# Optimization experiments

Measured on AMD Instinct MI355X. Metric: run time of the kernel, lower is better.

## Reference

```python
import jax, jax.numpy as jnp
import numpy as np

N_ENT = 200000
N_REL = 500
D_MODEL = 512
BS = 256


def setup_inputs() -> dict:
    key = jax.random.key(0)
    k1, k2, k3, k4, k5, k6 = jax.random.split(key, 6)
    return {
        "s_ent": jax.random.randint(k1, (BS,), 0, N_ENT, dtype=jnp.int32),
        "relation": jax.random.randint(k2, (BS,), 0, N_REL, dtype=jnp.int32),
        "o_ent": jax.random.randint(k3, (BS,), 0, N_ENT, dtype=jnp.int32),
        "time": jax.random.randint(k4, (BS,), 0, 365, dtype=jnp.int32),
        "ent_emb": jax.random.normal(k5, (N_ENT, D_MODEL), dtype=jnp.float32),
        "rel_emb": jax.random.normal(k6, (N_REL, D_MODEL), dtype=jnp.float32),
    }


def reference(s_ent, relation, o_ent, time, ent_emb, rel_emb):
    # test_forward: scores = -||(e_s + r) - E_all||_2 for every entity.
    # Faithful math via the ||a-b||^2 = ||a||^2 - 2 a.b + ||b||^2 GEMM
    # decomposition, avoiding the [bs, n_ent, d] difference tensor.
    cond = ent_emb[s_ent] + rel_emb[relation]          # [bs, d]
    a2 = jnp.sum(cond * cond, axis=-1, keepdims=True)  # [bs, 1]
    b2 = jnp.sum(ent_emb * ent_emb, axis=-1)           # [n_ent]
    ab = jnp.einsum('bd,nd->bn', cond, ent_emb)        # [bs, n_ent]
    d2 = a2 - 2.0 * ab + b2[None, :]
    scores = -jnp.sqrt(jnp.maximum(d2, 1e-12))
    return scores
```

## Files before the change

kernel.cpp:

```cpp
#include <hip/hip_runtime.h>
#include <hip/hip_bf16.h>

typedef __attribute__((ext_vector_type(8))) short short8;
typedef __attribute__((ext_vector_type(4))) float f32x4;

#define D_MODEL 512
#define BN 128
#define BK 32
#define NSTEPS (D_MODEL / BK)

__device__ inline short f2bf(float f) {
    unsigned u = __builtin_bit_cast(unsigned, f);
    unsigned r = (u + 0x7fffu + ((u >> 16) & 1u)) >> 16;
    return (short)r;
}

__global__ void prep_kernel(const int* __restrict__ s_ent, const int* __restrict__ rel,
                            const float* __restrict__ ent, const float* __restrict__ relemb,
                            short* __restrict__ condb, float* __restrict__ a2) {
    const int b = blockIdx.x;
    const int t = threadIdx.x;
    const float4 v = *(const float4*)(ent + (size_t)s_ent[b] * D_MODEL + t * 4);
    const float4 w = *(const float4*)(relemb + (size_t)rel[b] * D_MODEL + t * 4);
    float c0 = v.x + w.x, c1 = v.y + w.y, c2 = v.z + w.z, c3 = v.w + w.w;
    float sq = c0 * c0 + c1 * c1 + c2 * c2 + c3 * c3;

    short4 s;
    s.x = f2bf(c0); s.y = f2bf(c1); s.z = f2bf(c2); s.w = f2bf(c3);
    *(short4*)(condb + (size_t)b * D_MODEL + t * 4) = s;

    #pragma unroll
    for (int off = 1; off < 64; off <<= 1) sq += __shfl_xor(sq, off);
    __shared__ float red[2];
    if ((t & 63) == 0) red[t >> 6] = sq;
    __syncthreads();
    if (t == 0) a2[b] = red[0] + red[1];
}

__global__ __launch_bounds__(512, 4)
void score_kernel(const float* __restrict__ ent, const short* __restrict__ condb,
                  const float* __restrict__ a2, float* __restrict__ out, const int n_ent) {
    __shared__ __align__(16) short Bl[2][BN * 40];
    __shared__ float b2s[BN];

    const int tid  = threadIdx.x;
    const int lane = tid & 63;
    const int w    = tid >> 6;
    const int wm   = w >> 1;
    const int wn   = w & 1;
    const int lrow = lane & 15;
    const int lk   = (lane >> 4) * 8;
    const int nbase = blockIdx.x * BN;

    const int sr = tid >> 2;
    const int sk = (tid & 3) * 8;
    const bool rvalid = (nbase + sr) < n_ent;
    const float* gsrc = ent + (size_t)(nbase + sr) * D_MODEL + sk;

    f32x4 acc[4][4] = {};
    float sq = 0.f;

    float4 p0 = {0.f, 0.f, 0.f, 0.f}, p1 = {0.f, 0.f, 0.f, 0.f};
    if (rvalid) { p0 = *(const float4*)(gsrc); p1 = *(const float4*)(gsrc + 4); }

    #pragma unroll 2
    for (int t = 0; t < NSTEPS; ++t) {
        sq += p0.x * p0.x + p0.y * p0.y + p0.z * p0.z + p0.w * p0.w
            + p1.x * p1.x + p1.y * p1.y + p1.z * p1.z + p1.w * p1.w;
        short8 bs;
        bs[0] = f2bf(p0.x); bs[1] = f2bf(p0.y); bs[2] = f2bf(p0.z); bs[3] = f2bf(p0.w);
        bs[4] = f2bf(p1.x); bs[5] = f2bf(p1.y); bs[6] = f2bf(p1.z); bs[7] = f2bf(p1.w);
        *(short8*)(&Bl[t & 1][sr * 40 + sk]) = bs;

        if (t < NSTEPS - 1 && rvalid) {
            p0 = *(const float4*)(gsrc + (t + 1) * BK);
            p1 = *(const float4*)(gsrc + (t + 1) * BK + 4);
        }

        __syncthreads();

        const short* abase = condb + (size_t)(wm * 64 + lrow) * D_MODEL + t * BK + lk;
        short8 af[4];
        #pragma unroll
        for (int fm = 0; fm < 4; ++fm) af[fm] = *(const short8*)(abase + fm * 16 * D_MODEL);

        #pragma unroll
        for (int fn = 0; fn < 4; ++fn) {
            short8 bfv = *(const short8*)(&Bl[t & 1][(wn * 64 + fn * 16 + lrow) * 40 + lk]);
            #pragma unroll
            for (int fm = 0; fm < 4; ++fm)
                acc[fm][fn] = __builtin_amdgcn_mfma_f32_16x16x32_bf16(af[fm], bfv, acc[fm][fn], 0, 0, 0);
        }
    }

    sq += __shfl_xor(sq, 1);
    sq += __shfl_xor(sq, 2);
    if ((tid & 3) == 0) b2s[sr] = sq;
    __syncthreads();

    #pragma unroll
    for (int fm = 0; fm < 4; ++fm) {
        const int m = wm * 64 + fm * 16 + (lane >> 4) * 4;
        const f32x4 a2v = *(const f32x4*)(a2 + m);
        #pragma unroll
        for (int fn = 0; fn < 4; ++fn) {
            const int nl = wn * 64 + fn * 16 + lrow;
            const int ng = nbase + nl;
            if (ng < n_ent) {
                const float b2v = b2s[nl];
                #pragma unroll
                for (int r = 0; r < 4; ++r) {
                    float d2 = a2v[r] - 2.f * acc[fm][fn][r] + b2v;
                    out[(size_t)(m + r) * n_ent + ng] = -sqrtf(fmaxf(d2, 1e-12f));
                }
            }
        }
    }
}

extern "C" void kernel_launch(void* const* d_in, const int* in_sizes, int n_in,
                              void* d_out, int out_size, void* d_ws, size_t ws_size,
                              hipStream_t stream) {
    const int*   s_ent  = (const int*)d_in[0];
    const int*   rel    = (const int*)d_in[1];
    const float* ent    = (const float*)d_in[4];
    const float* relemb = (const float*)d_in[5];
    float* out = (float*)d_out;

    const int bs    = in_sizes[0];
    const int n_ent = in_sizes[4] / D_MODEL;

    short* condb = (short*)d_ws;
    float* a2    = (float*)((char*)d_ws + (size_t)bs * D_MODEL * 2);

    prep_kernel<<<bs, 128, 0, stream>>>(s_ent, rel, ent, relemb, condb, a2);

    const int ntiles = (n_ent + BN - 1) / BN;
    score_kernel<<<ntiles, 512, 0, stream>>>(ent, condb, a2, out, n_ent);
}
```

Baseline: 202.1 us.

## Stream A and fp32 B tiles to LDS via async global_load_lds with multi-buffering

The score kernel now copies both the bf16 query tile and the raw fp32 entity tile straight from global memory into swizzled LDS with async global_load_lds. A is double-buffered and B is triple-buffered, and waits use explicit vmcnt counters so loads for later k-steps overlap the MFMA work. The bf16 conversion and the squared-norm accumulation move to after the LDS read, so each wave converts its own B fragments. This duplicates conversion work across the wm waves and raises LDS use to about 80KB per block, which likely lowers the number of resident blocks per CU.

```diff
diff --git a/kernel.cpp b/kernel.cpp
--- a/kernel.cpp
+++ b/kernel.cpp
@@ -6,10 +6,17 @@
 
 #define D_MODEL 512
 #define BN 128
-#define BK 32
-#define NSTEPS (D_MODEL / BK)
+#define NT 16
+#define A_TILE 16384
+#define B_TILE 16384
 
-__device__ inline short f2bf(float f) {
+__device__ __forceinline__ void gload16(const void* gptr, void* lptr) {
+    typedef const __attribute__((address_space(1))) unsigned GT;
+    typedef __attribute__((address_space(3))) unsigned LT;
+    __builtin_amdgcn_global_load_lds((GT*)gptr, (LT*)lptr, 16, 0, 0);
+}
+
+__device__ __forceinline__ short f2bf(float f) {
     unsigned u = __builtin_bit_cast(unsigned, f);
     unsigned r = (u + 0x7fffu + ((u >> 16) & 1u)) >> 16;
     return (short)r;
@@ -40,68 +47,106 @@
 __global__ __launch_bounds__(512, 4)
 void score_kernel(const float* __restrict__ ent, const short* __restrict__ condb,
                   const float* __restrict__ a2, float* __restrict__ out, const int n_ent) {
-    __shared__ __align__(16) short Bl[2][BN * 40];
-    __shared__ float b2s[BN];
+    __shared__ __align__(16) unsigned char lds[2 * A_TILE + 3 * B_TILE];
+    unsigned char* Al = lds;
+    unsigned char* Bl = lds + 2 * A_TILE;
 
     const int tid  = threadIdx.x;
     const int lane = tid & 63;
-    const int w    = tid >> 6;
-    const int wm   = w >> 1;
-    const int wn   = w & 1;
-    const int lrow = lane & 15;
-    const int lk   = (lane >> 4) * 8;
+    const int w    = tid >> 6, wm = w >> 1, wn = w & 1;
+    const int lrow = lane & 15, g4 = lane >> 4;
     const int nbase = blockIdx.x * BN;
 
-    const int sr = tid >> 2;
-    const int sk = (tid & 3) * 8;
-    const bool rvalid = (nbase + sr) < n_ent;
-    const float* gsrc = ent + (size_t)(nbase + sr) * D_MODEL + sk;
+    const int p0 = tid * 16, p1 = p0 + 8192;
+    const int ar0 = p0 >> 6, ar1 = p1 >> 6;
+    const char* gA0 = (const char*)condb + ar0 * 1024 + ((p0 & 63) ^ ((ar0 & 3) << 4));
+    const char* gA1 = (const char*)condb + ar1 * 1024 + ((p1 & 63) ^ ((ar1 & 3) << 4));
+    const int br0 = p0 >> 7, br1 = p1 >> 7;
+    const long long gr0 = min(nbase + br0, n_ent - 1);
+    const long long gr1 = min(nbase + br1, n_ent - 1);
+    const char* gB0 = (const char*)ent + gr0 * 2048 + ((p0 & 127) ^ ((br0 & 7) << 4));
+    const char* gB1 = (const char*)ent + gr1 * 2048 + ((p1 & 127) ^ ((br1 & 7) << 4));
+
+    int aoff[4], boff0[4], boff1[4];
+    #pragma unroll
+    for (int f = 0; f < 4; ++f) {
+        const int ra = wm * 64 + f * 16 + lrow;
+        aoff[f] = ra * 64 + ((g4 * 16) ^ ((ra & 3) << 4));
+        const int rb = wn * 64 + f * 16 + lrow;
+        const int sw = (rb & 7) << 4;
+        boff0[f] = rb * 128 + ((g4 * 32) ^ sw);
+        boff1[f] = rb * 128 + ((g4 * 32 + 16) ^ sw);
+    }
 
     f32x4 acc[4][4] = {};
-    float sq = 0.f;
+    float sq[4] = {0.f, 0.f, 0.f, 0.f};
 
-    float4 p0 = {0.f, 0.f, 0.f, 0.f}, p1 = {0.f, 0.f, 0.f, 0.f};
-    if (rvalid) { p0 = *(const float4*)(gsrc); p1 = *(const float4*)(gsrc + 4); }
+    gload16(gA0, Al + p0);
+    gload16(gA1, Al + p1);
+    gload16(gB0, Bl + p0);
+    gload16(gB1, Bl + p1);
+    gload16(gB0 + 128, Bl + B_TILE + p0);
+    gload16(gB1 + 128, Bl + B_TILE + p1);
 
-    #pragma unroll 2
-    for (int t = 0; t < NSTEPS; ++t) {
-        sq += p0.x * p0.x + p0.y * p0.y + p0.z * p0.z + p0.w * p0.w
-            + p1.x * p1.x + p1.y * p1.y + p1.z * p1.z + p1.w * p1.w;
-        short8 bs;
-        bs[0] = f2bf(p0.x); bs[1] = f2bf(p0.y); bs[2] = f2bf(p0.z); bs[3] = f2bf(p0.w);
-        bs[4] = f2bf(p1.x); bs[5] = f2bf(p1.y); bs[6] = f2bf(p1.z); bs[7] = f2bf(p1.w);
-        *(short8*)(&Bl[t & 1][sr * 40 + sk]) = bs;
+    for (int t = 0; t < NT; ++t) {
+        if (t == NT - 1) { asm volatile("s_waitcnt vmcnt(0)" ::: "memory"); }
+        else             { asm volatile("s_waitcnt vmcnt(2)" ::: "memory"); }
+        __builtin_amdgcn_s_barrier();
 
-        if (t < NSTEPS - 1 && rvalid) {
-            p0 = *(const float4*)(gsrc + (t + 1) * BK);
-            p1 = *(const float4*)(gsrc + (t + 1) * BK + 4);
+        if (t + 1 < NT) {
+            unsigned char* ad = Al + ((t + 1) & 1) * A_TILE;
+            gload16(gA0 + (t + 1) * 64, ad + p0);
+            gload16(gA1 + (t + 1) * 64, ad + p1);
+        }
+        if (t + 2 < NT) {
+            unsigned char* bd = Bl + ((t + 2) % 3) * B_TILE;
+            gload16(gB0 + (t + 2) * 128, bd + p0);
+            gload16(gB1 + (t + 2) * 128, bd + p1);
         }
 
-        __syncthreads();
+        const unsigned char* ab = Al + (t & 1) * A_TILE;
+        const unsigned char* bb = Bl + (t % 3) * B_TILE;
 
-        const short* abase = condb + (size_t)(wm * 64 + lrow) * D_MODEL + t * BK + lk;
         short8 af[4];
         #pragma unroll
-        for (int fm = 0; fm < 4; ++fm) af[fm] = *(const short8*)(abase + fm * 16 * D_MODEL);
+        for (int fm = 0; fm < 4; ++fm) af[fm] = *(const short8*)(ab + aoff[fm]);
 
         #pragma unroll
         for (int fn = 0; fn < 4; ++fn) {
-            short8 bfv = *(const short8*)(&Bl[t & 1][(wn * 64 + fn * 16 + lrow) * 40 + lk]);
+            const f32x4 v0 = *(const f32x4*)(bb + boff0[fn]);
+            const f32x4 v1 = *(const f32x4*)(bb + boff1[fn]);
+            if (wm == 0)
+                sq[fn] += v0[0]*v0[0] + v0[1]*v0[1] + v0[2]*v0[2] + v0[3]*v0[3]
+                        + v1[0]*v1[0] + v1[1]*v1[1] + v1[2]*v1[2] + v1[3]*v1[3];
+            union { __hip_bfloat162 h[4]; short8 s; } cv;
+            cv.h[0] = __float22bfloat162_rn(make_float2(v0[0], v0[1]));
+            cv.h[1] = __float22bfloat162_rn(make_float2(v0[2], v0[3]));
+            cv.h[2] = __float22bfloat162_rn(make_float2(v1[0], v1[1]));
+            cv.h[3] = __float22bfloat162_rn(make_float2(v1[2], v1[3]));
             #pragma unroll
             for (int fm = 0; fm < 4; ++fm)
-                acc[fm][fn] = __builtin_amdgcn_mfma_f32_16x16x32_bf16(af[fm], bfv, acc[fm][fn], 0, 0, 0);
+                acc[fm][fn] = __builtin_amdgcn_mfma_f32_16x16x32_bf16(af[fm], cv.s, acc[fm][fn], 0, 0, 0);
         }
     }
 
-    sq += __shfl_xor(sq, 1);
-    sq += __shfl_xor(sq, 2);
-    if ((tid & 3) == 0) b2s[sr] = sq;
+    float* b2s = (float*)lds;
+    if (wm == 0) {
+        #pragma unroll
+        for (int fn = 0; fn < 4; ++fn) {
+            sq[fn] += __shfl_xor(sq[fn], 16);
+            sq[fn] += __shfl_xor(sq[fn], 32);
+        }
+        if (lane < 16) {
+            #pragma unroll
+            for (int fn = 0; fn < 4; ++fn) b2s[wn * 64 + fn * 16 + lane] = sq[fn];
+        }
+    }
     __syncthreads();
 
     #pragma unroll
     for (int fm = 0; fm < 4; ++fm) {
-        const int m = wm * 64 + fm * 16 + (lane >> 4) * 4;
-        const f32x4 a2v = *(const f32x4*)(a2 + m);
+        const int m0 = wm * 64 + fm * 16 + g4 * 4;
+        const f32x4 a2v = *(const f32x4*)(a2 + m0);
         #pragma unroll
         for (int fn = 0; fn < 4; ++fn) {
             const int nl = wn * 64 + fn * 16 + lrow;
@@ -111,7 +156,7 @@
                 #pragma unroll
                 for (int r = 0; r < 4; ++r) {
                     float d2 = a2v[r] - 2.f * acc[fm][fn][r] + b2v;
-                    out[(size_t)(m + r) * n_ent + ng] = -sqrtf(fmaxf(d2, 1e-12f));
+                    out[(size_t)(m0 + r) * n_ent + ng] = -sqrtf(fmaxf(d2, 1e-12f));
                 }
             }
         }
```

After: 164.6 us. -18.6%, faster.

## Stage A tile via global_load_lds with swizzled LDS and deeper B prefetch

Applied to the files above, without the earlier changes.

Stages the bf16 condition matrix into LDS using direct global-to-LDS loads instead of having each wave fetch it from global memory every k-step. The entity rows are prefetched two k-steps ahead in registers, and B is stored in an XOR-swizzled LDS layout instead of the padded one. The k-loop is hand-unrolled with explicit waitcnt and barrier placement to overlap loads, conversion and MFMA work. The larger LDS footprint (48 KB per block) may reduce how many blocks fit on each CU. The b2 reduction buffer now reuses the tile LDS space.

```diff
diff --git a/kernel.cpp b/kernel.cpp
--- a/kernel.cpp
+++ b/kernel.cpp
@@ -6,13 +6,33 @@
 
 #define D_MODEL 512
 #define BN 128
-#define BK 32
-#define NSTEPS (D_MODEL / BK)
+#define NT 16
+#define A_TILE 16384
+#define B_TILE 8192
 
-__device__ inline short f2bf(float f) {
+__device__ __forceinline__ void gload16(const void* g, void* l) {
+    typedef const __attribute__((address_space(1))) unsigned GT;
+    typedef __attribute__((address_space(3))) unsigned LT;
+    __builtin_amdgcn_global_load_lds((GT*)g, (LT*)l, 16, 0, 0);
+}
+
+__device__ __forceinline__ short f2bf(float f) {
     unsigned u = __builtin_bit_cast(unsigned, f);
     unsigned r = (u + 0x7fffu + ((u >> 16) & 1u)) >> 16;
     return (short)r;
+}
+
+__device__ __forceinline__ short8 cvt8(const float4& a, const float4& b) {
+    union { __hip_bfloat162 h[4]; short8 s; } u;
+    u.h[0] = __float22bfloat162_rn(make_float2(a.x, a.y));
+    u.h[1] = __float22bfloat162_rn(make_float2(a.z, a.w));
+    u.h[2] = __float22bfloat162_rn(make_float2(b.x, b.y));
+    u.h[3] = __float22bfloat162_rn(make_float2(b.z, b.w));
+    return u.s;
+}
+__device__ __forceinline__ float ssq(const float4& a, const float4& b) {
+    return a.x*a.x + a.y*a.y + a.z*a.z + a.w*a.w
+         + b.x*b.x + b.y*b.y + b.z*b.z + b.w*b.w;
 }
 
 __global__ void prep_kernel(const int* __restrict__ s_ent, const int* __restrict__ rel,
@@ -40,68 +60,88 @@
 __global__ __launch_bounds__(512, 4)
 void score_kernel(const float* __restrict__ ent, const short* __restrict__ condb,
                   const float* __restrict__ a2, float* __restrict__ out, const int n_ent) {
-    __shared__ __align__(16) short Bl[2][BN * 40];
-    __shared__ float b2s[BN];
+    __shared__ __align__(16) unsigned char lds[2 * A_TILE + 2 * B_TILE];
+    unsigned char* Al = lds;
+    unsigned char* Bl = lds + 2 * A_TILE;
 
     const int tid  = threadIdx.x;
     const int lane = tid & 63;
-    const int w    = tid >> 6;
-    const int wm   = w >> 1;
-    const int wn   = w & 1;
-    const int lrow = lane & 15;
-    const int lk   = (lane >> 4) * 8;
+    const int w    = tid >> 6, wm = w >> 1, wn = w & 1;
+    const int lrow = lane & 15, g4 = lane >> 4;
     const int nbase = blockIdx.x * BN;
 
-    const int sr = tid >> 2;
-    const int sk = (tid & 3) * 8;
-    const bool rvalid = (nbase + sr) < n_ent;
-    const float* gsrc = ent + (size_t)(nbase + sr) * D_MODEL + sk;
+    const int p0 = tid * 16, p1 = p0 + 8192;
+    const int ar0 = p0 >> 6, ar1 = p1 >> 6;
+    const char* gA0 = (const char*)condb + ar0 * 1024 + ((p0 & 63) ^ ((ar0 & 3) << 4));
+    const char* gA1 = (const char*)condb + ar1 * 1024 + ((p1 & 63) ^ ((ar1 & 3) << 4));
+
+    const int sr = tid >> 2, sk = (tid & 3) * 8;
+    const long long gr = min((long long)(nbase + sr), (long long)(n_ent - 1));
+    const float* gB = ent + gr * D_MODEL + sk;
+    const int bwoff = sr * 64 + ((sk * 2) ^ ((sr & 3) << 4));
+
+    const int base_a = (wm * 64 + lrow) * 64 + ((g4 * 16) ^ ((lrow & 3) << 4));
+    const int base_b = (wn * 64 + lrow) * 64 + ((g4 * 16) ^ ((lrow & 3) << 4));
 
     f32x4 acc[4][4] = {};
     float sq = 0.f;
 
-    float4 p0 = {0.f, 0.f, 0.f, 0.f}, p1 = {0.f, 0.f, 0.f, 0.f};
-    if (rvalid) { p0 = *(const float4*)(gsrc); p1 = *(const float4*)(gsrc + 4); }
+    float4 rbA0 = *(const float4*)(gB);
+    float4 rbA1 = *(const float4*)(gB + 4);
+    float4 rbB0 = *(const float4*)(gB + 32);
+    float4 rbB1 = *(const float4*)(gB + 36);
+    gload16(gA0, Al + p0);
+    gload16(gA1, Al + p1);
+    sq += ssq(rbA0, rbA1);
+    *(short8*)(Bl + bwoff) = cvt8(rbA0, rbA1);
 
-    #pragma unroll 2
-    for (int t = 0; t < NSTEPS; ++t) {
-        sq += p0.x * p0.x + p0.y * p0.y + p0.z * p0.z + p0.w * p0.w
-            + p1.x * p1.x + p1.y * p1.y + p1.z * p1.z + p1.w * p1.w;
-        short8 bs;
-        bs[0] = f2bf(p0.x); bs[1] = f2bf(p0.y); bs[2] = f2bf(p0.z); bs[3] = f2bf(p0.w);
-        bs[4] = f2bf(p1.x); bs[5] = f2bf(p1.y); bs[6] = f2bf(p1.z); bs[7] = f2bf(p1.w);
-        *(short8*)(&Bl[t & 1][sr * 40 + sk]) = bs;
+#define KSTEP(T, CV0, CV1, LD0, LD1, DO_CVT, DO_LDB, DO_LDA)                              \
+  {                                                                                        \
+    asm volatile("s_waitcnt vmcnt(0)" ::: "memory");                                       \
+    short8 cb;                                                                             \
+    if (DO_CVT) { sq += ssq(CV0, CV1); cb = cvt8(CV0, CV1); }                              \
+    asm volatile("s_waitcnt lgkmcnt(0)" ::: "memory");                                     \
+    __builtin_amdgcn_s_barrier();                                                          \
+    if (DO_LDB) { LD0 = *(const float4*)(gB + ((T) + 2) * 32);                             \
+                  LD1 = *(const float4*)(gB + ((T) + 2) * 32 + 4); }                       \
+    if (DO_LDA) { unsigned char* ad = Al + (((T) + 1) & 1) * A_TILE;                       \
+                  gload16(gA0 + ((T) + 1) * 64, ad + p0);                                  \
+                  gload16(gA1 + ((T) + 1) * 64, ad + p1); }                                \
+    if (DO_CVT) *(short8*)(Bl + (((T) + 1) & 1) * B_TILE + bwoff) = cb;                    \
+    const unsigned char* ab = Al + ((T) & 1) * A_TILE;                                     \
+    const unsigned char* bb = Bl + ((T) & 1) * B_TILE;                                     \
+    short8 af0 = *(const short8*)(ab + base_a);                                            \
+    short8 af1 = *(const short8*)(ab + base_a + 1024);                                     \
+    short8 af2 = *(const short8*)(ab + base_a + 2048);                                     \
+    short8 af3 = *(const short8*)(ab + base_a + 3072);                                     \
+    _Pragma("unroll")                                                                      \
+    for (int fn = 0; fn < 4; ++fn) {                                                       \
+      short8 bf = *(const short8*)(bb + base_b + fn * 1024);                               \
+      acc[0][fn] = __builtin_amdgcn_mfma_f32_16x16x32_bf16(af0, bf, acc[0][fn], 0, 0, 0);  \
+      acc[1][fn] = __builtin_amdgcn_mfma_f32_16x16x32_bf16(af1, bf, acc[1][fn], 0, 0, 0);  \
+      acc[2][fn] = __builtin_amdgcn_mfma_f32_16x16x32_bf16(af2, bf, acc[2][fn], 0, 0, 0);  \
+      acc[3][fn] = __builtin_amdgcn_mfma_f32_16x16x32_bf16(af3, bf, acc[3][fn], 0, 0, 0);  \
+    }                                                                                      \
+  }
 
-        if (t < NSTEPS - 1 && rvalid) {
-            p0 = *(const float4*)(gsrc + (t + 1) * BK);
-            p1 = *(const float4*)(gsrc + (t + 1) * BK + 4);
-        }
-
-        __syncthreads();
-
-        const short* abase = condb + (size_t)(wm * 64 + lrow) * D_MODEL + t * BK + lk;
-        short8 af[4];
-        #pragma unroll
-        for (int fm = 0; fm < 4; ++fm) af[fm] = *(const short8*)(abase + fm * 16 * D_MODEL);
-
-        #pragma unroll
-        for (int fn = 0; fn < 4; ++fn) {
-            short8 bfv = *(const short8*)(&Bl[t & 1][(wn * 64 + fn * 16 + lrow) * 40 + lk]);
-            #pragma unroll
-            for (int fm = 0; fm < 4; ++fm)
-                acc[fm][fn] = __builtin_amdgcn_mfma_f32_16x16x32_bf16(af[fm], bfv, acc[fm][fn], 0, 0, 0);
-        }
+    for (int tt = 0; tt < 14; tt += 2) {
+        KSTEP(tt,     rbB0, rbB1, rbA0, rbA1, true,  true,  true)
+        KSTEP(tt + 1, rbA0, rbA1, rbB0, rbB1, true,  true,  true)
     }
+    KSTEP(14, rbB0, rbB1, rbA0, rbA1, true,  false, true)
+    KSTEP(15, rbA0, rbA1, rbB0, rbB1, false, false, false)
+#undef KSTEP
 
     sq += __shfl_xor(sq, 1);
     sq += __shfl_xor(sq, 2);
+    float* b2s = (float*)lds;
     if ((tid & 3) == 0) b2s[sr] = sq;
     __syncthreads();
 
     #pragma unroll
     for (int fm = 0; fm < 4; ++fm) {
-        const int m = wm * 64 + fm * 16 + (lane >> 4) * 4;
-        const f32x4 a2v = *(const f32x4*)(a2 + m);
+        const int m0 = wm * 64 + fm * 16 + g4 * 4;
+        const f32x4 a2v = *(const f32x4*)(a2 + m0);
         #pragma unroll
         for (int fn = 0; fn < 4; ++fn) {
             const int nl = wn * 64 + fn * 16 + lrow;
@@ -111,7 +151,7 @@
                 #pragma unroll
                 for (int r = 0; r < 4; ++r) {
                     float d2 = a2v[r] - 2.f * acc[fm][fn][r] + b2v;
-                    out[(size_t)(m + r) * n_ent + ng] = -sqrtf(fmaxf(d2, 1e-12f));
+                    out[(size_t)(m0 + r) * n_ent + ng] = -sqrtf(fmaxf(d2, 1e-12f));
                 }
             }
         }
```

New measurement: 173.7 us. 14.1% less time.

## Stage whole entity tile in swizzled LDS once, drop K-loop barriers

Applied to the files above, without the earlier changes.

The score kernel now uses 64-entity tiles. Each block issues all sixteen global loads per thread up front, converts the full 512-wide rows to bf16 with a packed conversion intrinsic, and writes them into an XOR-swizzled LDS buffer behind a single barrier. The MFMA loop then runs over K with no per-step synchronisation, and each wave covers 32 query rows across all 64 entities. This removes sixteen barriers and the serialized load/convert/compute pipeline, at the cost of 64KB of LDS per block, which can limit occupancy, and about twice as many A-fragment reloads from global memory per output.

```diff
diff --git a/kernel.cpp b/kernel.cpp
--- a/kernel.cpp
+++ b/kernel.cpp
@@ -5,14 +5,20 @@
 typedef __attribute__((ext_vector_type(4))) float f32x4;
 
 #define D_MODEL 512
-#define BN 128
-#define BK 32
-#define NSTEPS (D_MODEL / BK)
+#define BN 64
+#define NPASS 16
 
-__device__ inline short f2bf(float f) {
+__device__ __forceinline__ short f2bf(float f) {
     unsigned u = __builtin_bit_cast(unsigned, f);
     unsigned r = (u + 0x7fffu + ((u >> 16) & 1u)) >> 16;
     return (short)r;
+}
+
+__device__ __forceinline__ short4 cvt4(const float4& v) {
+    union { __hip_bfloat162 h[2]; short4 s; } u;
+    u.h[0] = __float22bfloat162_rn(make_float2(v.x, v.y));
+    u.h[1] = __float22bfloat162_rn(make_float2(v.z, v.w));
+    return u.s;
 }
 
 __global__ void prep_kernel(const int* __restrict__ s_ent, const int* __restrict__ rel,
@@ -40,78 +46,72 @@
 __global__ __launch_bounds__(512, 4)
 void score_kernel(const float* __restrict__ ent, const short* __restrict__ condb,
                   const float* __restrict__ a2, float* __restrict__ out, const int n_ent) {
-    __shared__ __align__(16) short Bl[2][BN * 40];
+    __shared__ __align__(16) short Bp[BN * D_MODEL];
     __shared__ float b2s[BN];
 
     const int tid  = threadIdx.x;
     const int lane = tid & 63;
     const int w    = tid >> 6;
-    const int wm   = w >> 1;
-    const int wn   = w & 1;
-    const int lrow = lane & 15;
-    const int lk   = (lane >> 4) * 8;
-    const int nbase = blockIdx.x * BN;
+    const int lrow = lane & 15, g4 = lane >> 4;
+    const long long nbase = (long long)blockIdx.x * BN;
 
-    const int sr = tid >> 2;
-    const int sk = (tid & 3) * 8;
-    const bool rvalid = (nbase + sr) < n_ent;
-    const float* gsrc = ent + (size_t)(nbase + sr) * D_MODEL + sk;
+    const char* gent = (const char*)ent;
+    float4 stg[NPASS];
+    #pragma unroll
+    for (int p = 0; p < NPASS; ++p) {
+        const long long grow = min(nbase + w * 8 + (p >> 1), (long long)(n_ent - 1));
+        stg[p] = *(const float4*)(gent + grow * 2048 + (p & 1) * 1024 + lane * 16);
+    }
+    float sqp[8];
+    #pragma unroll
+    for (int r = 0; r < 8; ++r) sqp[r] = 0.f;
+    #pragma unroll
+    for (int p = 0; p < NPASS; ++p) {
+        const int row = w * 8 + (p >> 1);
+        const int cb  = (p & 1) * 512 + lane * 8;
+        const float4 v = stg[p];
+        sqp[p >> 1] += v.x * v.x + v.y * v.y + v.z * v.z + v.w * v.w;
+        *(short4*)((char*)Bp + row * 1024 + (cb ^ ((row & 7) << 4))) = cvt4(v);
+    }
+    #pragma unroll
+    for (int r = 0; r < 8; ++r) {
+        float s = sqp[r];
+        #pragma unroll
+        for (int off = 1; off < 64; off <<= 1) s += __shfl_xor(s, off);
+        if (lane == 0) b2s[w * 8 + r] = s;
+    }
+    __syncthreads();
 
-    f32x4 acc[4][4] = {};
-    float sq = 0.f;
+    const short* abase = condb + (size_t)(w * 32 + lrow) * D_MODEL + g4 * 8;
 
-    float4 p0 = {0.f, 0.f, 0.f, 0.f}, p1 = {0.f, 0.f, 0.f, 0.f};
-    if (rvalid) { p0 = *(const float4*)(gsrc); p1 = *(const float4*)(gsrc + 4); }
-
-    #pragma unroll 2
-    for (int t = 0; t < NSTEPS; ++t) {
-        sq += p0.x * p0.x + p0.y * p0.y + p0.z * p0.z + p0.w * p0.w
-            + p1.x * p1.x + p1.y * p1.y + p1.z * p1.z + p1.w * p1.w;
-        short8 bs;
-        bs[0] = f2bf(p0.x); bs[1] = f2bf(p0.y); bs[2] = f2bf(p0.z); bs[3] = f2bf(p0.w);
-        bs[4] = f2bf(p1.x); bs[5] = f2bf(p1.y); bs[6] = f2bf(p1.z); bs[7] = f2bf(p1.w);
-        *(short8*)(&Bl[t & 1][sr * 40 + sk]) = bs;
-
-        if (t < NSTEPS - 1 && rvalid) {
-            p0 = *(const float4*)(gsrc + (t + 1) * BK);
-            p1 = *(const float4*)(gsrc + (t + 1) * BK + 4);
-        }
-
-        __syncthreads();
-
-        const short* abase = condb + (size_t)(wm * 64 + lrow) * D_MODEL + t * BK + lk;
-        short8 af[4];
-        #pragma unroll
-        for (int fm = 0; fm < 4; ++fm) af[fm] = *(const short8*)(abase + fm * 16 * D_MODEL);
-
+    f32x4 acc[2][4] = {};
+    #pragma unroll
+    for (int t = 0; t < 16; ++t) {
+        const short8 af0 = *(const short8*)(abase + t * 32);
+        const short8 af1 = *(const short8*)(abase + t * 32 + 16 * D_MODEL);
         #pragma unroll
         for (int fn = 0; fn < 4; ++fn) {
-            short8 bfv = *(const short8*)(&Bl[t & 1][(wn * 64 + fn * 16 + lrow) * 40 + lk]);
-            #pragma unroll
-            for (int fm = 0; fm < 4; ++fm)
-                acc[fm][fn] = __builtin_amdgcn_mfma_f32_16x16x32_bf16(af[fm], bfv, acc[fm][fn], 0, 0, 0);
+            const int rb = fn * 16 + lrow;
+            const short8 bf = *(const short8*)((const char*)Bp + rb * 1024 +
+                                               ((t * 64 + g4 * 16) ^ ((rb & 7) << 4)));
+            acc[0][fn] = __builtin_amdgcn_mfma_f32_16x16x32_bf16(af0, bf, acc[0][fn], 0, 0, 0);
+            acc[1][fn] = __builtin_amdgcn_mfma_f32_16x16x32_bf16(af1, bf, acc[1][fn], 0, 0, 0);
         }
     }
 
-    sq += __shfl_xor(sq, 1);
-    sq += __shfl_xor(sq, 2);
-    if ((tid & 3) == 0) b2s[sr] = sq;
-    __syncthreads();
-
     #pragma unroll
-    for (int fm = 0; fm < 4; ++fm) {
-        const int m = wm * 64 + fm * 16 + (lane >> 4) * 4;
-        const f32x4 a2v = *(const f32x4*)(a2 + m);
+    for (int fm = 0; fm < 2; ++fm) {
+        const int m0 = w * 32 + fm * 16 + g4 * 4;
+        const f32x4 a2v = *(const f32x4*)(a2 + m0);
         #pragma unroll
         for (int fn = 0; fn < 4; ++fn) {
-            const int nl = wn * 64 + fn * 16 + lrow;
-            const int ng = nbase + nl;
+            const long long ng = nbase + fn * 16 + lrow;
             if (ng < n_ent) {
-                const float b2v = b2s[nl];
+                const float b2v = b2s[fn * 16 + lrow];
                 #pragma unroll
                 for (int r = 0; r < 4; ++r) {
                     float d2 = a2v[r] - 2.f * acc[fm][fn][r] + b2v;
-                    out[(size_t)(m + r) * n_ent + ng] = -sqrtf(fmaxf(d2, 1e-12f));
+                    out[(size_t)(m0 + r) * n_ent + ng] = -sqrtf(fmaxf(d2, 1e-12f));
                 }
             }
         }
```

After: 210.5 us. 1.04x slower.
